# Kernel tuning notes

Measured on AMD Instinct MI355X. Metric: run time of the kernel, lower is better.

## Reference

```python
import jax, jax.numpy as jnp
import numpy as np

EPS = 1e-5

def _ada_ln(x, t, W, b):
    # NOTE: original code defines SiLU but never applies it in forward -> faithful: plain linear.
    emb = t @ W + b                       # (b, 1, 2*dim)
    scale, shift = jnp.split(emb, 2, axis=-1)
    mu = x.mean(-1, keepdims=True)
    var = ((x - mu) ** 2).mean(-1, keepdims=True)
    xn = (x - mu) * jax.lax.rsqrt(var + EPS)   # LayerNorm, elementwise_affine=False
    return xn * (1.0 + scale) + shift

def _attn(x, ctx, Wq, Wk, Wv, Wo, bo, heads):
    b, n, _ = x.shape
    j = ctx.shape[1]
    q = (x @ Wq).reshape(b, n, heads, -1)      # (b, i, h, dh)
    k = (ctx @ Wk).reshape(b, j, heads, -1)
    v = (ctx @ Wv).reshape(b, j, heads, -1)
    scale = q.shape[-1] ** -0.5
    sim = jnp.einsum('bihd,bjhd->bhij', q, k) * scale
    attn = jax.nn.softmax(sim, axis=-1)
    out = jnp.einsum('bhij,bjhd->bihd', attn, v).reshape(b, n, -1)
    return out @ Wo + bo

def _ff(x, W1, b1, W2, b2):
    p = x @ W1 + b1                            # (b, n, 8*dim)
    a, gate = jnp.split(p, 2, axis=-1)
    return (a * jax.nn.gelu(gate, approximate=False)) @ W2 + b2

def setup_inputs() -> dict:
    key = jax.random.key(0)
    ks = jax.random.split(key, 32)
    B, N, D = 4, 2048, 1024
    J, CD = 256, 768
    H, DH = 16, 64
    INNER = H * DH           # 1024
    FF = 4 * D               # 4096
    w = lambda k, shp: jax.random.normal(k, shp, jnp.float32) * 0.02
    inp = {
        'x': jax.random.normal(ks[0], (B, N, D), jnp.float32),
        't': jax.random.normal(ks[1], (B, 1, D), jnp.float32),
        'context': jax.random.normal(ks[2], (B, J, CD), jnp.float32),
        # AdaLayerNorms (weights stored (in, out))
        'n1_w': w(ks[3], (D, 2 * D)), 'n1_b': jnp.zeros((2 * D,), jnp.float32),
        'n2_w': w(ks[4], (D, 2 * D)), 'n2_b': jnp.zeros((2 * D,), jnp.float32),
        'n3_w': w(ks[5], (D, 2 * D)), 'n3_b': jnp.zeros((2 * D,), jnp.float32),
        # attn1 (self)
        'q1': w(ks[6], (D, INNER)), 'k1': w(ks[7], (D, INNER)), 'v1': w(ks[8], (D, INNER)),
        'o1_w': w(ks[9], (INNER, D)), 'o1_b': jnp.zeros((D,), jnp.float32),
        # attn2 (cross)
        'q2': w(ks[10], (D, INNER)), 'k2': w(ks[11], (CD, INNER)), 'v2': w(ks[12], (CD, INNER)),
        'o2_w': w(ks[13], (INNER, D)), 'o2_b': jnp.zeros((D,), jnp.float32),
        # GEGLU FeedForward
        'ff_w1': w(ks[14], (D, 2 * FF)), 'ff_b1': jnp.zeros((2 * FF,), jnp.float32),
        'ff_w2': w(ks[15], (FF, D)), 'ff_b2': jnp.zeros((D,), jnp.float32),
    }
    return inp

def reference(x, t, context,
              n1_w, n1_b, n2_w, n2_b, n3_w, n3_b,
              q1, k1, v1, o1_w, o1_b,
              q2, k2, v2, o2_w, o2_b,
              ff_w1, ff_b1, ff_w2, ff_b2):
    H = 16
    h = _ada_ln(x, t, n1_w, n1_b)
    x = _attn(h, h, q1, k1, v1, o1_w, o1_b, H) + x
    h = _ada_ln(x, t, n2_w, n2_b)
    x = _attn(h, context, q2, k2, v2, o2_w, o2_b, H) + x
    h = _ada_ln(x, t, n3_w, n3_b)
    x = _ff(h, ff_w1, ff_b1, ff_w2, ff_b2) + x
    return x
```

## Files before the change

kernel.cpp:

```cpp
#include <hip/hip_runtime.h>
#include <hip/hip_bf16.h>
#include <stdint.h>

typedef unsigned short u16;
typedef __attribute__((ext_vector_type(8))) short bf16x8;
typedef __attribute__((ext_vector_type(4))) float f32x4;

__device__ __forceinline__ u16 f2bf(float f) {
  __hip_bfloat16 h = __float2bfloat16(f);
  return *reinterpret_cast<u16*>(&h);
}
__device__ __forceinline__ float bf2f(u16 v) {
  return __uint_as_float(((uint32_t)v) << 16);
}
__device__ __forceinline__ float exp2_fast(float x) {
  return __builtin_amdgcn_exp2f(x);
}

typedef __attribute__((address_space(1))) const uint32_t gu32;
typedef __attribute__((address_space(3))) uint32_t lu32;
__device__ __forceinline__ void gload16(const u16* g, u16* l) {
  __builtin_amdgcn_global_load_lds((gu32*)g, (lu32*)l, 16, 0, 0);
}

__device__ __forceinline__ int2 block_mn(int colsz) {
  int nwg = gridDim.x * gridDim.y, nby = gridDim.y;
  int id = blockIdx.y * gridDim.x + blockIdx.x;
  int swz = (nwg & 7) ? id : ((id & 7) * (nwg >> 3) + (id >> 3));
  return make_int2((swz % nby) * 128, (swz / nby) * colsz);
}

__global__ __launch_bounds__(256)
void wtrans_k(const float* __restrict__ W, u16* __restrict__ Wt, int K, int N) {
  __shared__ float tile[32][33];
  int n0 = blockIdx.x * 32, k0 = blockIdx.y * 32;
  int t = threadIdx.x;
  int c = t & 31, r4 = t >> 5;
#pragma unroll
  for (int s = 0; s < 4; ++s) {
    int kr = r4 + 8 * s;
    tile[kr][c] = W[(size_t)(k0 + kr) * N + n0 + c];
  }
  __syncthreads();
#pragma unroll
  for (int s = 0; s < 4; ++s) {
    int nr = r4 + 8 * s;
    Wt[(size_t)(n0 + nr) * K + k0 + c] = f2bf(tile[c][nr]);
  }
}

__global__ __launch_bounds__(256)
void cvt_bf16_k(const float* __restrict__ in, u16* __restrict__ out, int n4) {
  int i = blockIdx.x * 256 + threadIdx.x;
  if (i < n4) {
    float4 v = ((const float4*)in)[i];
    ushort4 o;
    o.x = f2bf(v.x); o.y = f2bf(v.y); o.z = f2bf(v.z); o.w = f2bf(v.w);
    ((ushort4*)out)[i] = o;
  }
}

__global__ __launch_bounds__(256)
void vtrans_k(const u16* __restrict__ V, int sv, u16* __restrict__ Vt, int Nkv) {
  __shared__ u16 Tl[64][72];
  const int bh = blockIdx.y, b = bh >> 4, hh = bh & 15;
  const int jt = blockIdx.x, t = threadIdx.x;
  const int ntile = Nkv >> 6;
  {
    int jr = t >> 2, part = t & 3;
    const u16* src = V + (size_t)(b * Nkv + jt * 64 + jr) * sv + hh * 64 + part * 16;
    *(uint4*)(&Tl[jr][part * 16]) = *(const uint4*)src;
    *(uint4*)(&Tl[jr][part * 16 + 8]) = *(const uint4*)(src + 8);
  }
  __syncthreads();
  int d = t >> 2, ch = t & 3;
  u16 ov[16];
#pragma unroll
  for (int e = 0; e < 16; ++e) {
    int jj = ch * 16 + e;
    ov[e] = Tl[jj ^ ((d & 7) << 3)][d];
  }
  u16* dst = Vt + ((size_t)bh * ntile + jt) * 4096 + d * 64 + ch * 16;
  *(uint4*)dst = *(uint4*)&ov[0];
  *(uint4*)(dst + 8) = *(uint4*)&ov[8];
}

__global__ __launch_bounds__(256)
void emb_all_k(const float* __restrict__ tin,
               const float* __restrict__ w0, const float* __restrict__ b0,
               const float* __restrict__ w1, const float* __restrict__ b1,
               const float* __restrict__ w2, const float* __restrict__ b2,
               float* __restrict__ emb) {
  int p = blockIdx.x >> 5, c = blockIdx.x & 31;
  int norm = p >> 2, b = p & 3;
  int t = threadIdx.x;
  int n = c * 64 + (t & 63), kc = t >> 6;
  const float* W = norm == 0 ? w0 : (norm == 1 ? w1 : w2);
  const float* Bv = norm == 0 ? b0 : (norm == 1 ? b1 : b2);
  const float* tr = tin + b * 1024 + kc * 256;
  const float* Wp = W + (size_t)(kc * 256) * 2048 + n;
  float acc = 0.f;
#pragma unroll 8
  for (int k = 0; k < 256; ++k) acc = fmaf(tr[k], Wp[(size_t)k * 2048], acc);
  __shared__ float red[256];
  red[t] = acc;
  __syncthreads();
  if (kc == 0)
    emb[p * 2048 + n] = red[t] + red[64 + t] + red[128 + t] + red[192 + t] + Bv[n];
}

__global__ __launch_bounds__(256)
void ada_ln_k(const float* __restrict__ x, const float* __restrict__ emb,
              u16* __restrict__ h) {
  int row = blockIdx.x;
  int b = row >> 11;
  int t = threadIdx.x;
  const float4* xr = (const float4*)(x + (size_t)row * 1024);
  float4 v = xr[t];
  float s = v.x + v.y + v.z + v.w;
  float s2 = v.x * v.x + v.y * v.y + v.z * v.z + v.w * v.w;
#pragma unroll
  for (int m = 1; m < 64; m <<= 1) { s += __shfl_xor(s, m); s2 += __shfl_xor(s2, m); }
  __shared__ float rs[4], rs2[4];
  int w = t >> 6;
  if ((t & 63) == 0) { rs[w] = s; rs2[w] = s2; }
  __syncthreads();
  s = rs[0] + rs[1] + rs[2] + rs[3];
  s2 = rs2[0] + rs2[1] + rs2[2] + rs2[3];
  float mu = s * (1.f / 1024.f);
  float var = s2 * (1.f / 1024.f) - mu * mu;
  float rstd = rsqrtf(var + 1e-5f);
  const float4* sc = (const float4*)(emb + b * 2048);
  const float4* sh = (const float4*)(emb + b * 2048 + 1024);
  float4 c = sc[t], f = sh[t];
  ushort4 o;
  o.x = f2bf((v.x - mu) * rstd * (1.f + c.x) + f.x);
  o.y = f2bf((v.y - mu) * rstd * (1.f + c.y) + f.y);
  o.z = f2bf((v.z - mu) * rstd * (1.f + c.z) + f.z);
  o.w = f2bf((v.w - mu) * rstd * (1.f + c.w) + f.w);
  ((ushort4*)(h + (size_t)row * 1024))[t] = o;
}

enum { EPI_BF16 = 0, EPI_BIAS_RES = 1, EPI_GEGLU = 2, EPI_QKV = 3 };
#define QSCALE 0.1803368801111244f

template <int EPI>
__device__ __forceinline__ void epi_store(float v, int col, size_t idx,
                                          u16* outb, float* outf,
                                          const float* res) {
  if (EPI == EPI_BF16) {
    outb[idx] = f2bf(v);
  } else if (EPI == EPI_QKV) {
    outb[idx] = f2bf(col < 1024 ? v * QSCALE : v);
  } else if (EPI == EPI_BIAS_RES) {
    outf[idx] = v + res[idx];
  }
}

template <int EPI>
__global__ __launch_bounds__(256)
void gemm_k(const u16* __restrict__ A, int lda,
            const u16* __restrict__ Bt, int ldb,
            const float* __restrict__ bias,
            const float* __restrict__ res,
            u16* __restrict__ outb, float* __restrict__ outf,
            int N, int K) {
  __shared__ u16 As[2][128 * 32];
  __shared__ u16 Bs[2][128 * 32];
  int2 mn = block_mn(128);
  const int m0 = mn.x, n0 = mn.y;
  const int t = threadIdx.x;
  const int l = t & 63, w = t >> 6, lg = l >> 4, li = l & 15;
  const int wm = w >> 1, wn = w & 1;
  const int c0 = w, c1 = w + 4;
  const int r0 = c0 * 16 + (l >> 2), r1 = c1 * 16 + (l >> 2);
  const int cc = (l & 3) * 8;
  const u16* ga0 = A + (size_t)(m0 + r0) * lda + cc;
  const u16* ga1 = A + (size_t)(m0 + r1) * lda + cc;
  const u16* gb0 = Bt + (size_t)(n0 + r0) * ldb + cc;
  const u16* gb1 = Bt + (size_t)(n0 + r1) * ldb + cc;
  f32x4 acc[4][4] = {};
  auto stage = [&](int p, int k0) {
    gload16(ga0 + k0, As[p] + c0 * 512);
    gload16(ga1 + k0, As[p] + c1 * 512);
    gload16(gb0 + k0, Bs[p] + c0 * 512);
    gload16(gb1 + k0, Bs[p] + c1 * 512);
  };
  stage(0, 0);
  __syncthreads();
  int p = 0;
  for (int k0 = 0; k0 < K; k0 += 32) {
    if (k0 + 32 < K) stage(p ^ 1, k0 + 32);
    bf16x8 af[4], bfr[4];
#pragma unroll
    for (int i = 0; i < 4; ++i) {
      af[i]  = *(const bf16x8*)(As[p] + (wm * 64 + i * 16 + li) * 32 + lg * 8);
      bfr[i] = *(const bf16x8*)(Bs[p] + (wn * 64 + i * 16 + li) * 32 + lg * 8);
    }
#pragma unroll
    for (int i = 0; i < 4; ++i)
#pragma unroll
      for (int j = 0; j < 4; ++j)
        acc[i][j] = __builtin_amdgcn_mfma_f32_16x16x32_bf16(af[i], bfr[j], acc[i][j], 0, 0, 0);
    __syncthreads();
    p ^= 1;
  }
#pragma unroll
  for (int j = 0; j < 4; ++j) {
    int col = n0 + wn * 64 + j * 16 + li;
    float bv = bias ? bias[col] : 0.f;
#pragma unroll
    for (int i = 0; i < 4; ++i) {
#pragma unroll
      for (int r = 0; r < 4; ++r) {
        int row = m0 + wm * 64 + i * 16 + lg * 4 + r;
        size_t idx = (size_t)row * N + col;
        epi_store<EPI>(acc[i][j][r] + bv, col, idx, outb, outf, res);
      }
    }
  }
}

template <int EPI>
__global__ __launch_bounds__(512)
void gemm2_k(const u16* __restrict__ A, int lda,
             const u16* __restrict__ Bt, int ldb, int roff2,
             const float* __restrict__ bias,
             u16* __restrict__ outb, int N, int K) {
  __shared__ u16 As[2][4096];
  __shared__ u16 B0s[2][4096];
  __shared__ u16 B1s[2][4096];
  int2 mn = block_mn(EPI == EPI_QKV ? 256 : 128);
  const int m0 = mn.x, n0 = mn.y;
  const int t = threadIdx.x;
  const int w = t >> 6, l = t & 63, lg = l >> 4, li = l & 15;
  const int wm = w >> 2, wn = w & 3;
  const int sr = (w << 4) + (l >> 2), sc = (l & 3) * 8;
  const u16* ga  = A  + (size_t)(m0 + sr) * lda + sc;
  const u16* gb0 = Bt + (size_t)(n0 + sr) * ldb + sc;
  const u16* gb1 = Bt + (size_t)(n0 + roff2 + sr) * ldb + sc;
  const int ldst = w * 512;
  f32x4 acc0[4][2] = {}, acc1[4][2] = {};
  auto stage = [&](int p, int k0) {
    gload16(ga + k0, As[p] + ldst);
    gload16(gb0 + k0, B0s[p] + ldst);
    gload16(gb1 + k0, B1s[p] + ldst);
  };
  stage(0, 0);
  __syncthreads();
  int p = 0;
  for (int k0 = 0; k0 < K; k0 += 32) {
    if (k0 + 32 < K) stage(p ^ 1, k0 + 32);
    bf16x8 af[4], b0[2], b1[2];
#pragma unroll
    for (int i = 0; i < 4; ++i)
      af[i] = *(const bf16x8*)(As[p] + (wm * 64 + i * 16 + li) * 32 + lg * 8);
#pragma unroll
    for (int j = 0; j < 2; ++j) {
      b0[j] = *(const bf16x8*)(B0s[p] + (wn * 32 + j * 16 + li) * 32 + lg * 8);
      b1[j] = *(const bf16x8*)(B1s[p] + (wn * 32 + j * 16 + li) * 32 + lg * 8);
    }
#pragma unroll
    for (int i = 0; i < 4; ++i)
#pragma unroll
      for (int j = 0; j < 2; ++j) {
        acc0[i][j] = __builtin_amdgcn_mfma_f32_16x16x32_bf16(af[i], b0[j], acc0[i][j], 0, 0, 0);
        acc1[i][j] = __builtin_amdgcn_mfma_f32_16x16x32_bf16(af[i], b1[j], acc1[i][j], 0, 0, 0);
      }
    __syncthreads();
    p ^= 1;
  }
#pragma unroll
  for (int j = 0; j < 2; ++j) {
    int cw = wn * 32 + j * 16 + li;
    if (EPI == EPI_QKV) {
#pragma unroll
      for (int sub = 0; sub < 2; ++sub) {
        int col = n0 + sub * 128 + cw;
#pragma unroll
        for (int i = 0; i < 4; ++i)
#pragma unroll
          for (int r = 0; r < 4; ++r) {
            int row = m0 + wm * 64 + i * 16 + lg * 4 + r;
            float v = sub ? acc1[i][j][r] : acc0[i][j][r];
            outb[(size_t)row * N + col] = f2bf(col < 1024 ? v * QSCALE : v);
          }
      }
    } else {
      int col = n0 + cw;
      float ba = bias[col], bg = bias[col + roff2];
#pragma unroll
      for (int i = 0; i < 4; ++i)
#pragma unroll
        for (int r = 0; r < 4; ++r) {
          int row = m0 + wm * 64 + i * 16 + lg * 4 + r;
          float a = acc0[i][j][r] + ba;
          float g = acc1[i][j][r] + bg;
          float gl = 0.5f * g * (1.0f + erff(g * 0.70710678118f));
          outb[(size_t)row * N + col] = f2bf(a * gl);
        }
    }
  }
}

__global__ __launch_bounds__(512)
void flash_k(const u16* __restrict__ Q, int sq, const u16* __restrict__ Kb, int skv,
             const u16* __restrict__ Vt, u16* __restrict__ O,
             int Nq, int Nkv) {
  __shared__ u16 Kl[2][4096];
  __shared__ u16 Vl[2][4096];
  __shared__ u16 Pl[8][16][72];
  const int t = threadIdx.x, w = t >> 6, l = t & 63, lg = l >> 4, li = l & 15;
  const int bh = blockIdx.y, b = bh >> 4, hh = bh & 15;
  const int i0 = blockIdx.x * 256;
  const int ntile = Nkv >> 6;
  const u16* qrow0 = Q + ((size_t)b * Nq + i0 + w * 32 + li) * sq + hh * 64;
  const u16* qrow1 = qrow0 + (size_t)16 * sq;
  bf16x8 qf[2][2];
  qf[0][0] = *(const bf16x8*)(qrow0 + lg * 8);
  qf[0][1] = *(const bf16x8*)(qrow0 + 32 + lg * 8);
  qf[1][0] = *(const bf16x8*)(qrow1 + lg * 8);
  qf[1][1] = *(const bf16x8*)(qrow1 + 32 + lg * 8);
  const int krow_in = l >> 3;
  const int kcol = ((l & 7) ^ (l >> 3)) * 8;
  const u16* kbase = Kb + (size_t)b * Nkv * skv + hh * 64 + kcol;
  const u16* vtb = Vt + ((size_t)bh * ntile) * 4096 + l * 8;
  f32x4 sden[2] = {};
  f32x4 of[2][4] = {};
  bf16x8 ones;
#pragma unroll
  for (int e = 0; e < 8; ++e) ones[e] = (short)0x3F80;
  int kx[2], vx[2];
#pragma unroll
  for (int hf = 0; hf < 2; ++hf)
    kx[hf] = ((hf * 64 + lg * 16) ^ ((li & 7) << 4)) >> 1;
#pragma unroll
  for (int ks = 0; ks < 2; ++ks)
    vx[ks] = (ks * 32 + lg * 8) ^ ((li & 7) << 3);
  const int px = (lg * 8) ^ (((li >> 3) & 1) << 3);
  auto stage = [&](int p, int jt) {
    gload16(kbase + (size_t)(jt * 64 + w * 8 + krow_in) * skv, Kl[p] + w * 512);
    gload16(vtb + (size_t)jt * 4096 + w * 512, Vl[p] + w * 512);
  };
  stage(0, 0);
  __syncthreads();
  int p = 0;
  for (int jt = 0; jt < ntile; ++jt) {
    if (jt + 1 < ntile) stage(p ^ 1, jt + 1);
    const u16* Kp = Kl[p] + li * 64;
    const u16* Vp = Vl[p] + li * 64;
#pragma unroll
    for (int q = 0; q < 2; ++q) {
      f32x4 sacc[4] = {};
      __builtin_amdgcn_s_setprio(1);
#pragma unroll
      for (int nt = 0; nt < 4; ++nt) {
        bf16x8 k0 = *(const bf16x8*)(Kp + nt * 1024 + kx[0]);
        bf16x8 k1 = *(const bf16x8*)(Kp + nt * 1024 + kx[1]);
        sacc[nt] = __builtin_amdgcn_mfma_f32_16x16x32_bf16(qf[q][0], k0, sacc[nt], 0, 0, 0);
        sacc[nt] = __builtin_amdgcn_mfma_f32_16x16x32_bf16(qf[q][1], k1, sacc[nt], 0, 0, 0);
      }
      __builtin_amdgcn_s_setprio(0);
#pragma unroll
      for (int nt = 0; nt < 4; ++nt)
#pragma unroll
        for (int r = 0; r < 4; ++r) {
          float pe = exp2_fast(fminf(sacc[nt][r], 60.f));
          int prow = lg * 4 + r;
          Pl[w][prow][(nt * 16 + li) ^ (((prow >> 3) & 1) << 3)] = f2bf(pe);
        }
      __builtin_amdgcn_s_setprio(1);
#pragma unroll
      for (int ks = 0; ks < 2; ++ks) {
        bf16x8 pa = *(const bf16x8*)(&Pl[w][li][ks * 32 + px]);
#pragma unroll
        for (int nt = 0; nt < 4; ++nt) {
          bf16x8 vf = *(const bf16x8*)(Vp + nt * 1024 + vx[ks]);
          of[q][nt] = __builtin_amdgcn_mfma_f32_16x16x32_bf16(pa, vf, of[q][nt], 0, 0, 0);
        }
        sden[q] = __builtin_amdgcn_mfma_f32_16x16x32_bf16(pa, ones, sden[q], 0, 0, 0);
      }
      __builtin_amdgcn_s_setprio(0);
    }
    __syncthreads();
    p ^= 1;
  }
#pragma unroll
  for (int q = 0; q < 2; ++q)
#pragma unroll
    for (int r = 0; r < 4; ++r) {
      float inv = 1.f / sden[q][r];
      int row = i0 + w * 32 + q * 16 + lg * 4 + r;
      u16* orow = O + ((size_t)b * Nq + row) * 1024 + hh * 64;
#pragma unroll
      for (int nt = 0; nt < 4; ++nt)
        orow[nt * 16 + li] = f2bf(of[q][nt][r] * inv);
    }
}

extern "C" void kernel_launch(void* const* d_in, const int* in_sizes, int n_in,
                              void* d_out, int out_size, void* d_ws, size_t ws_size,
                              hipStream_t stream) {
  const float* X   = (const float*)d_in[0];
  const float* T   = (const float*)d_in[1];
  const float* CTX = (const float*)d_in[2];
  const float* N1W = (const float*)d_in[3];
  const float* N1B = (const float*)d_in[4];
  const float* N2W = (const float*)d_in[5];
  const float* N2B = (const float*)d_in[6];
  const float* N3W = (const float*)d_in[7];
  const float* N3B = (const float*)d_in[8];
  const float* Q1  = (const float*)d_in[9];
  const float* K1  = (const float*)d_in[10];
  const float* V1  = (const float*)d_in[11];
  const float* O1W = (const float*)d_in[12];
  const float* O1B = (const float*)d_in[13];
  const float* Q2  = (const float*)d_in[14];
  const float* K2  = (const float*)d_in[15];
  const float* V2  = (const float*)d_in[16];
  const float* O2W = (const float*)d_in[17];
  const float* O2B = (const float*)d_in[18];
  const float* FW1 = (const float*)d_in[19];
  const float* FB1 = (const float*)d_in[20];
  const float* FW2 = (const float*)d_in[21];
  const float* FB2 = (const float*)d_in[22];
  float* OUT = (float*)d_out;

  char* ws = (char*)d_ws;
  const size_t MB = 1ull << 20;
  u16* wt_q1 = (u16*)(ws + 0 * MB);
  u16* wt_k1 = (u16*)(ws + 2 * MB);
  u16* wt_v1 = (u16*)(ws + 4 * MB);
  u16* wt_o1 = (u16*)(ws + 6 * MB);
  u16* wt_q2 = (u16*)(ws + 8 * MB);
  u16* wt_k2 = (u16*)(ws + 10 * MB);
  u16* wt_v2 = (u16*)(ws + 10 * MB + 1536 * 1024);
  u16* wt_o2 = (u16*)(ws + 13 * MB);
  u16* wt_f1 = (u16*)(ws + 16 * MB);
  u16* wt_f2 = (u16*)(ws + 32 * MB);
  u16* ctxb  = (u16*)(ws + 40 * MB);
  float* emb = (float*)(ws + 42 * MB);
  u16* hbuf  = (u16*)(ws + 43 * MB);
  u16* vtbuf = (u16*)(ws + 43 * MB);
  u16* QKVb  = (u16*)(ws + 59 * MB);
  u16* Qb    = (u16*)(ws + 59 * MB);
  u16* KVb   = (u16*)(ws + 75 * MB);
  u16* AOb   = (u16*)(ws + 107 * MB);
  u16* abuf  = (u16*)(ws + 59 * MB);

  wtrans_k<<<dim3(32, 32), 256, 0, stream>>>(Q1, wt_q1, 1024, 1024);
  wtrans_k<<<dim3(32, 32), 256, 0, stream>>>(K1, wt_k1, 1024, 1024);
  wtrans_k<<<dim3(32, 32), 256, 0, stream>>>(V1, wt_v1, 1024, 1024);
  wtrans_k<<<dim3(32, 32), 256, 0, stream>>>(O1W, wt_o1, 1024, 1024);
  wtrans_k<<<dim3(32, 32), 256, 0, stream>>>(Q2, wt_q2, 1024, 1024);
  wtrans_k<<<dim3(32, 24), 256, 0, stream>>>(K2, wt_k2, 768, 1024);
  wtrans_k<<<dim3(32, 24), 256, 0, stream>>>(V2, wt_v2, 768, 1024);
  wtrans_k<<<dim3(32, 32), 256, 0, stream>>>(O2W, wt_o2, 1024, 1024);
  wtrans_k<<<dim3(256, 32), 256, 0, stream>>>(FW1, wt_f1, 1024, 8192);
  wtrans_k<<<dim3(32, 128), 256, 0, stream>>>(FW2, wt_f2, 4096, 1024);
  cvt_bf16_k<<<768, 256, 0, stream>>>(CTX, ctxb, 196608);
  emb_all_k<<<384, 256, 0, stream>>>(T, N1W, N1B, N2W, N2B, N3W, N3B, emb);

  ada_ln_k<<<8192, 256, 0, stream>>>(X, emb + 0, hbuf);
  gemm2_k<EPI_QKV><<<dim3(12, 64), 512, 0, stream>>>(hbuf, 1024, wt_q1, 1024, 128, nullptr, QKVb, 3072, 1024);
  vtrans_k<<<dim3(32, 64), 256, 0, stream>>>(QKVb + 2048, 3072, vtbuf, 2048);
  flash_k<<<dim3(8, 64), 512, 0, stream>>>(QKVb, 3072, QKVb + 1024, 3072, vtbuf, AOb, 2048, 2048);
  gemm_k<EPI_BIAS_RES><<<dim3(8, 64), 256, 0, stream>>>(AOb, 1024, wt_o1, 1024, O1B, X, nullptr, OUT, 1024, 1024);

  ada_ln_k<<<8192, 256, 0, stream>>>(OUT, emb + 8192, hbuf);
  gemm_k<EPI_QKV><<<dim3(8, 64), 256, 0, stream>>>(hbuf, 1024, wt_q2, 1024, nullptr, nullptr, Qb, nullptr, 1024, 1024);
  gemm_k<EPI_BF16><<<dim3(16, 8), 256, 0, stream>>>(ctxb, 768, wt_k2, 768, nullptr, nullptr, KVb, nullptr, 2048, 768);
  vtrans_k<<<dim3(4, 64), 256, 0, stream>>>(KVb + 1024, 2048, vtbuf, 256);
  flash_k<<<dim3(8, 64), 512, 0, stream>>>(Qb, 1024, KVb, 2048, vtbuf, AOb, 2048, 256);
  gemm_k<EPI_BIAS_RES><<<dim3(8, 64), 256, 0, stream>>>(AOb, 1024, wt_o2, 1024, O2B, OUT, nullptr, OUT, 1024, 1024);

  ada_ln_k<<<8192, 256, 0, stream>>>(OUT, emb + 16384, hbuf);
  gemm2_k<EPI_GEGLU><<<dim3(32, 64), 512, 0, stream>>>(hbuf, 1024, wt_f1, 1024, 4096, FB1, abuf, 4096, 1024);
  gemm_k<EPI_BIAS_RES><<<dim3(8, 64), 256, 0, stream>>>(abuf, 4096, wt_f2, 4096, FB2, OUT, nullptr, OUT, 1024, 4096);
}
```

Measured before the change: 656.1 us.

## Route output, Q and FF2 projections through the wider dual-B gemm2 kernel

gemm2_k gains a column-size template parameter and a residual/float output path. It can now do bias+residual and Q-scale epilogues through epi_store, with two B tiles offset by roff2. The o1, q2, o2 and ff2 GEMMs switch from the 256-thread gemm_k to 512-thread gemm2_k blocks covering 128x256 outputs, halving the grid and improving A-tile reuse. The block-to-tile swizzle mapping also changes to derive rows from swz/nbx, which alters L2 traffic order for all gemm2 launches. The cost is fewer blocks per GEMM, 256 on a 256-CU part, so occupancy and tail balance may suffer.

```diff
diff --git a/kernel.cpp b/kernel.cpp
--- a/kernel.cpp
+++ b/kernel.cpp
@@ -24,10 +24,11 @@
 }
 
 __device__ __forceinline__ int2 block_mn(int colsz) {
-  int nwg = gridDim.x * gridDim.y, nby = gridDim.y;
-  int id = blockIdx.y * gridDim.x + blockIdx.x;
+  int nbx = gridDim.x;
+  int id = blockIdx.y * nbx + blockIdx.x;
+  int nwg = nbx * gridDim.y;
   int swz = (nwg & 7) ? id : ((id & 7) * (nwg >> 3) + (id >> 3));
-  return make_int2((swz % nby) * 128, (swz / nby) * colsz);
+  return make_int2((swz / nbx) * 128, (swz % nbx) * colsz);
 }
 
 __global__ __launch_bounds__(256)
@@ -221,16 +222,18 @@
   }
 }
 
-template <int EPI>
+template <int EPI, int COLSZ>
 __global__ __launch_bounds__(512)
 void gemm2_k(const u16* __restrict__ A, int lda,
              const u16* __restrict__ Bt, int ldb, int roff2,
              const float* __restrict__ bias,
-             u16* __restrict__ outb, int N, int K) {
+             const float* __restrict__ res,
+             u16* __restrict__ outb, float* __restrict__ outf,
+             int N, int K) {
   __shared__ u16 As[2][4096];
   __shared__ u16 B0s[2][4096];
   __shared__ u16 B1s[2][4096];
-  int2 mn = block_mn(EPI == EPI_QKV ? 256 : 128);
+  int2 mn = block_mn(COLSZ);
   const int m0 = mn.x, n0 = mn.y;
   const int t = threadIdx.x;
   const int w = t >> 6, l = t & 63, lg = l >> 4, li = l & 15;
@@ -273,20 +276,7 @@
 #pragma unroll
   for (int j = 0; j < 2; ++j) {
     int cw = wn * 32 + j * 16 + li;
-    if (EPI == EPI_QKV) {
-#pragma unroll
-      for (int sub = 0; sub < 2; ++sub) {
-        int col = n0 + sub * 128 + cw;
-#pragma unroll
-        for (int i = 0; i < 4; ++i)
-#pragma unroll
-          for (int r = 0; r < 4; ++r) {
-            int row = m0 + wm * 64 + i * 16 + lg * 4 + r;
-            float v = sub ? acc1[i][j][r] : acc0[i][j][r];
-            outb[(size_t)row * N + col] = f2bf(col < 1024 ? v * QSCALE : v);
-          }
-      }
-    } else {
+    if (EPI == EPI_GEGLU) {
       int col = n0 + cw;
       float ba = bias[col], bg = bias[col + roff2];
 #pragma unroll
@@ -299,6 +289,20 @@
           float gl = 0.5f * g * (1.0f + erff(g * 0.70710678118f));
           outb[(size_t)row * N + col] = f2bf(a * gl);
         }
+    } else {
+#pragma unroll
+      for (int sub = 0; sub < 2; ++sub) {
+        int col = n0 + sub * roff2 + cw;
+        float bv = bias ? bias[col] : 0.f;
+#pragma unroll
+        for (int i = 0; i < 4; ++i)
+#pragma unroll
+          for (int r = 0; r < 4; ++r) {
+            int row = m0 + wm * 64 + i * 16 + lg * 4 + r;
+            float v = (sub ? acc1[i][j][r] : acc0[i][j][r]) + bv;
+            epi_store<EPI>(v, col, (size_t)row * N + col, outb, outf, res);
+          }
+      }
     }
   }
 }
@@ -462,19 +466,19 @@
   emb_all_k<<<384, 256, 0, stream>>>(T, N1W, N1B, N2W, N2B, N3W, N3B, emb);
 
   ada_ln_k<<<8192, 256, 0, stream>>>(X, emb + 0, hbuf);
-  gemm2_k<EPI_QKV><<<dim3(12, 64), 512, 0, stream>>>(hbuf, 1024, wt_q1, 1024, 128, nullptr, QKVb, 3072, 1024);
+  gemm2_k<EPI_QKV, 256><<<dim3(12, 64), 512, 0, stream>>>(hbuf, 1024, wt_q1, 1024, 128, nullptr, nullptr, QKVb, nullptr, 3072, 1024);
   vtrans_k<<<dim3(32, 64), 256, 0, stream>>>(QKVb + 2048, 3072, vtbuf, 2048);
   flash_k<<<dim3(8, 64), 512, 0, stream>>>(QKVb, 3072, QKVb + 1024, 3072, vtbuf, AOb, 2048, 2048);
-  gemm_k<EPI_BIAS_RES><<<dim3(8, 64), 256, 0, stream>>>(AOb, 1024, wt_o1, 1024, O1B, X, nullptr, OUT, 1024, 1024);
+  gemm2_k<EPI_BIAS_RES, 128><<<dim3(4, 64), 512, 0, stream>>>(AOb, 1024, wt_o1, 1024, 512, O1B, X, nullptr, OUT, 1024, 1024);
 
   ada_ln_k<<<8192, 256, 0, stream>>>(OUT, emb + 8192, hbuf);
-  gemm_k<EPI_QKV><<<dim3(8, 64), 256, 0, stream>>>(hbuf, 1024, wt_q2, 1024, nullptr, nullptr, Qb, nullptr, 1024, 1024);
+  gemm2_k<EPI_QKV, 128><<<dim3(4, 64), 512, 0, stream>>>(hbuf, 1024, wt_q2, 1024, 512, nullptr, nullptr, Qb, nullptr, 1024, 1024);
   gemm_k<EPI_BF16><<<dim3(16, 8), 256, 0, stream>>>(ctxb, 768, wt_k2, 768, nullptr, nullptr, KVb, nullptr, 2048, 768);
   vtrans_k<<<dim3(4, 64), 256, 0, stream>>>(KVb + 1024, 2048, vtbuf, 256);
   flash_k<<<dim3(8, 64), 512, 0, stream>>>(Qb, 1024, KVb, 2048, vtbuf, AOb, 2048, 256);
-  gemm_k<EPI_BIAS_RES><<<dim3(8, 64), 256, 0, stream>>>(AOb, 1024, wt_o2, 1024, O2B, OUT, nullptr, OUT, 1024, 1024);
+  gemm2_k<EPI_BIAS_RES, 128><<<dim3(4, 64), 512, 0, stream>>>(AOb, 1024, wt_o2, 1024, 512, O2B, OUT, nullptr, OUT, 1024, 1024);
 
   ada_ln_k<<<8192, 256, 0, stream>>>(OUT, emb + 16384, hbuf);
-  gemm2_k<EPI_GEGLU><<<dim3(32, 64), 512, 0, stream>>>(hbuf, 1024, wt_f1, 1024, 4096, FB1, abuf, 4096, 1024);
-  gemm_k<EPI_BIAS_RES><<<dim3(8, 64), 256, 0, stream>>>(abuf, 4096, wt_f2, 4096, FB2, OUT, nullptr, OUT, 1024, 4096);
-}
+  gemm2_k<EPI_GEGLU, 128><<<dim3(32, 64), 512, 0, stream>>>(hbuf, 1024, wt_f1, 1024, 4096, FB1, nullptr, abuf, nullptr, 4096, 1024);
+  gemm2_k<EPI_BIAS_RES, 128><<<dim3(4, 64), 512, 0, stream>>>(abuf, 4096, wt_f2, 4096, 512, FB2, OUT, nullptr, OUT, 1024, 4096);
+}
```

Measured after the change: 697.7 us. 1.06x slower.
